# Performance work log

Measured on AMD Instinct MI355X. Metric: run time of the kernel, lower is better.

The kernel has to match this reference:

```python
import jax, jax.numpy as jnp
import numpy as np

SR = 24000
N_FFT = 2048
WIN = 960
HOP = 240
NUM_BANDS = 150
HID = 128
OUT = 64
LOG_E_MIN = -18.0  # stands in for trained log_energy_min buffer
LOG_E_MAX = 5.0    # stands in for trained log_energy_max buffer
FREQ_INTERVAL = SR / N_FFT


def _stft_power(x):
    # torchaudio Spectrogram(power=2, center=True, pad_mode=reflect)
    pad = N_FFT // 2
    xp = jnp.pad(x, ((0, 0), (pad, pad)), mode='reflect')
    n = jnp.arange(WIN, dtype=jnp.float32)
    win = 0.5 - 0.5 * jnp.cos(2.0 * jnp.pi * n / WIN)  # periodic hann
    lp = (N_FFT - WIN) // 2
    win = jnp.pad(win, (lp, N_FFT - WIN - lp))  # center-pad window to n_fft
    T = 1 + x.shape[1] // HOP
    idx = (jnp.arange(T) * HOP)[:, None] + jnp.arange(N_FFT)[None, :]  # [T, n_fft]
    frames = xp[:, idx] * win  # [B, T, n_fft]
    F = jnp.fft.rfft(frames, axis=-1)  # [B, T, n_fft//2+1]
    return F.real ** 2 + F.imag ** 2


def _lstm_dir(feat_tbd, w_ih, w_hh, b, reverse):
    # feat_tbd: [T, B, D]; PyTorch gate order i, f, g, o
    xs = jnp.flip(feat_tbd, 0) if reverse else feat_tbd
    pre = jnp.einsum('tbd,gd->tbg', xs, w_ih) + b  # input projection hoisted out of scan

    def step(carry, z_in):
        h, c = carry
        z = z_in + h @ w_hh.T
        i, f, g, o = jnp.split(z, 4, axis=-1)
        c = jax.nn.sigmoid(f) * c + jax.nn.sigmoid(i) * jnp.tanh(g)
        h = jax.nn.sigmoid(o) * jnp.tanh(c)
        return (h, c), h

    B = feat_tbd.shape[1]
    h0 = jnp.zeros((B, HID), feat_tbd.dtype)
    _, hs = jax.lax.scan(step, (h0, h0), pre)
    return jnp.flip(hs, 0) if reverse else hs


def setup_inputs() -> dict:
    key = jax.random.key(0)
    ks = jax.random.split(key, 12)
    B, L, T = 16, 240000, 1001
    x = jax.random.normal(ks[0], (B, L), jnp.float32) * 0.1
    f0_raw = jax.random.uniform(ks[1], (B, T), jnp.float32, 50.0, 400.0)
    voiced = jax.random.uniform(ks[2], (B, T)) > 0.1
    f0 = jnp.where(voiced, f0_raw, 0.0)
    D_in = NUM_BANDS * 2 + 1  # 301
    s = 0.08
    return {
        'x': x,
        'f0': f0,
        'w_ih_f': jax.random.normal(ks[3], (4 * HID, D_in), jnp.float32) * s,
        'w_hh_f': jax.random.normal(ks[4], (4 * HID, HID), jnp.float32) * s,
        'b_f': jax.random.normal(ks[5], (4 * HID,), jnp.float32) * s,
        'w_ih_b': jax.random.normal(ks[6], (4 * HID, D_in), jnp.float32) * s,
        'w_hh_b': jax.random.normal(ks[7], (4 * HID, HID), jnp.float32) * s,
        'b_b': jax.random.normal(ks[8], (4 * HID,), jnp.float32) * s,
        'ln_g': jnp.ones((2 * HID,), jnp.float32),
        'ln_b': jnp.zeros((2 * HID,), jnp.float32),
        'out_w': jax.random.normal(ks[9], (OUT, 2 * HID), jnp.float32) * 0.02,
        'out_b': jnp.zeros((OUT,), jnp.float32),
    }


def reference(x, f0, w_ih_f, w_hh_f, b_f, w_ih_b, w_hh_b, b_b, ln_g, ln_b, out_w, out_b):
    spec = _stft_power(x)                     # [B, T, 1025]
    spec = spec.at[..., -1].set(0.0)          # spec[..., -1] = 0
    Tf = min(spec.shape[1], f0.shape[1])
    spec = spec[:, :Tf]
    f0 = f0[:, :Tf]
    f0_nonzero = jnp.where(f0 > 0, f0, SR / NUM_BANDS * 0.5)
    mult = jnp.arange(1.0, NUM_BANDS + 0.5, 0.5, dtype=jnp.float32)  # [299]
    harms = f0_nonzero[..., None] * mult                              # [B, T, 299]
    harms = jnp.concatenate([harms[..., :1] * 0.5, harms], axis=-1)   # [B, T, 300]
    hidx = jnp.clip(jnp.round(harms / FREQ_INTERVAL).astype(jnp.int32), 0, spec.shape[-1] - 1)
    harms_energy = jnp.take_along_axis(spec, hidx, axis=-1)           # irregular gather
    log_energy = jnp.log(harms_energy + 1e-8)
    feature = (log_energy - LOG_E_MIN) / (LOG_E_MAX - LOG_E_MIN)
    feature = jnp.concatenate([feature, jnp.log(f0_nonzero)[..., None]], axis=-1)  # [B, T, 301]
    ft = feature.transpose(1, 0, 2)  # [T, B, 301]
    hf = _lstm_dir(ft, w_ih_f, w_hh_f, b_f, False)
    hb = _lstm_dir(ft, w_ih_b, w_hh_b, b_b, True)
    h = jnp.concatenate([hf, hb], axis=-1).transpose(1, 0, 2)  # [B, T, 256]
    mu = h.mean(-1, keepdims=True)
    var = h.var(-1, keepdims=True)
    hn = (h - mu) / jnp.sqrt(var + 1e-5) * ln_g + ln_b
    return hn @ out_w.T + out_b  # [B, T, 64]
```

## Files before the change

### kernel.cpp

```cpp
#include <hip/hip_runtime.h>

typedef __bf16 bf16x8 __attribute__((ext_vector_type(8)));
typedef float f32x4 __attribute__((ext_vector_type(4)));

__device__ __forceinline__ void sync_lds() {
    asm volatile("s_waitcnt lgkmcnt(0)" ::: "memory");
    __builtin_amdgcn_s_barrier();
}

__global__ __launch_bounds__(256) void prep_kernel(
    const float* __restrict__ x, const float* __restrict__ w_ih_f, const float* __restrict__ w_ih_b,
    __bf16* __restrict__ BT, __bf16* __restrict__ A, __bf16* __restrict__ WT)
{
    int blk = blockIdx.x;
    if (blk < 7680) {
        int id = blk * 256 + threadIdx.x;
        int n = id / 960;
        int j = id - n * 960;
        int k = n >> 1;
        int p = (k * (544 + j)) & 2047;
        float pr = (float)p * (1.0f / 2048.0f);
        float v = (n & 1) ? __builtin_amdgcn_sinf(pr) : __builtin_amdgcn_cosf(pr);
        BT[id] = (__bf16)v;
    } else if (blk < 37920) {
        int id = (blk - 7680) * 256 + threadIdx.x;
        int frame = id / 480;
        int jp = (id - frame * 480) * 2;
        float v[2] = {0.f, 0.f};
        if (frame < 16016) {
            int b = frame / 1001;
            int t = frame - b * 1001;
            const float* xb = x + (size_t)b * 240000;
            #pragma unroll
            for (int e = 0; e < 2; ++e) {
                int j = jp + e;
                int s = t * 240 + j - 480;
                if (s < 0) s = -s;
                else if (s >= 240000) s = 479998 - s;
                float win = 0.5f - 0.5f * __builtin_amdgcn_cosf((float)j * (1.0f / 960.0f));
                v[e] = xb[s] * win;
            }
        }
        union { unsigned int u; __bf16 h[2]; } pk;
        pk.h[0] = (__bf16)v[0]; pk.h[1] = (__bf16)v[1];
        *reinterpret_cast<unsigned int*>(&A[(size_t)frame * 960 + jp]) = pk.u;
    } else {
        int id = (blk - 37920) * 256 + threadIdx.x;
        int n = id / 320;
        int k = id - n * 320;
        float v = 0.f;
        if (k < 301) v = (n < 512) ? w_ih_f[n * 301 + k] : w_ih_b[(n - 512) * 301 + k];
        WT[id] = (__bf16)v;
    }
}

__global__ __launch_bounds__(256) void gemm_kernel(
    const __bf16* __restrict__ A, const __bf16* __restrict__ BT,
    int Ka, int kIters, int mode,
    __bf16* __restrict__ Cdft, float* __restrict__ pre,
    const float* __restrict__ b_f, const float* __restrict__ b_b)
{
    __shared__ __bf16 As[128 * 64];
    __shared__ __bf16 Bs[128 * 64];
    const int tid = threadIdx.x;
    const int wave = tid >> 6, lane = tid & 63, l15 = lane & 15, quad = lane >> 4;
    const int bn = blockIdx.x, bm = blockIdx.y;
    const int qm = wave >> 1, qn = wave & 1;
    f32x4 acc[4][4] = {};
    const int rl  = lane >> 3;
    const int gch = (lane & 7) ^ rl;
    const __bf16* Ag = A + (size_t)(bm * 128) * Ka;
    const __bf16* Bg = BT + (size_t)(bn * 128) * Ka;

    for (int kb = 0; kb < kIters; ++kb) {
        int k0 = kb * 64;
        #pragma unroll
        for (int p = 0; p < 4; ++p) {
            int c = wave + p * 4;
            int row = c * 8 + rl;
            __builtin_amdgcn_global_load_lds(
                (const __attribute__((address_space(1))) void*)(Ag + (size_t)row * Ka + k0 + gch * 8),
                (__attribute__((address_space(3))) void*)(As + c * 512), 16, 0, 0);
            __builtin_amdgcn_global_load_lds(
                (const __attribute__((address_space(1))) void*)(Bg + (size_t)row * Ka + k0 + gch * 8),
                (__attribute__((address_space(3))) void*)(Bs + c * 512), 16, 0, 0);
        }
        __syncthreads();
        #pragma unroll
        for (int ks = 0; ks < 2; ++ks) {
            bf16x8 af[4], bfr[4];
            #pragma unroll
            for (int i = 0; i < 4; ++i) {
                int row = qm * 64 + i * 16 + l15;
                int ch = (ks * 4 + quad) ^ (l15 & 7);
                af[i] = *reinterpret_cast<const bf16x8*>(&As[row * 64 + ch * 8]);
            }
            #pragma unroll
            for (int j = 0; j < 4; ++j) {
                int row = qn * 64 + j * 16 + l15;
                int ch = (ks * 4 + quad) ^ (l15 & 7);
                bfr[j] = *reinterpret_cast<const bf16x8*>(&Bs[row * 64 + ch * 8]);
            }
            #pragma unroll
            for (int i = 0; i < 4; ++i)
                #pragma unroll
                for (int j = 0; j < 4; ++j)
                    acc[i][j] = __builtin_amdgcn_mfma_f32_16x16x32_bf16(af[i], bfr[j], acc[i][j], 0, 0, 0);
        }
        __syncthreads();
    }

    if (mode == 0) {
        #pragma unroll
        for (int i = 0; i < 4; ++i)
            #pragma unroll
            for (int j = 0; j < 4; ++j) {
                int n = bn * 128 + qn * 64 + j * 16 + l15;
                #pragma unroll
                for (int r = 0; r < 4; ++r) {
                    int m = bm * 128 + qm * 64 + i * 16 + quad * 4 + r;
                    Cdft[(size_t)m * 2048 + n] = (__bf16)acc[i][j][r];
                }
            }
    } else {
        for (int i = 0; i < 4; ++i)
            for (int j = 0; j < 4; ++j) {
                int n = bn * 128 + qn * 64 + j * 16 + l15;
                float bias = (n < 512) ? b_f[n] : b_b[n - 512];
                int dirg = n >> 9;
                int ngate = n & 511;
                int g = ngate >> 7;
                int jj = ngate & 127;
                for (int r = 0; r < 4; ++r) {
                    int m = bm * 128 + qm * 64 + i * 16 + quad * 4 + r;
                    if (m < 16016) {
                        int b = m / 1001;
                        int t = m - b * 1001;
                        size_t off = ((size_t)(t * 2 + dirg) * 16 + b) * 512 + jj * 4 + g;
                        pre[off] = acc[i][j][r] + bias;
                    }
                }
            }
    }
}

__global__ __launch_bounds__(256) void build_feat(const float* __restrict__ f0,
    const __bf16* __restrict__ Cdft, __bf16* __restrict__ feat)
{
    __shared__ __bf16 row[2048];
    const int frame = blockIdx.x;
    const int tid = threadIdx.x;
    __builtin_amdgcn_global_load_lds(
        (const __attribute__((address_space(1))) void*)(Cdft + (size_t)frame * 2048 + tid * 8),
        (__attribute__((address_space(3))) void*)(row + (tid >> 6) * 512), 16, 0, 0);

    int b = frame / 1001;
    int t = frame - b * 1001;
    float f0v = f0[b * 1001 + t];
    float f0nz = (f0v > 0.f) ? f0v : 80.f;
    __syncthreads();

    const float LN2 = 0.6931471805599453f;
    for (int d = tid; d < 320; d += 256) {
        float val = 0.f;
        if (d < 300) {
            float mult = (d == 0) ? 0.5f : (float)(d + 1) * 0.5f;
            int kidx = (int)rintf(f0nz * mult * (1.0f / 11.71875f));
            kidx = min(max(kidx, 0), 1024);
            float e = 0.f;
            if (kidx < 1024) {
                union { unsigned int u; __bf16 h[2]; } c;
                c.u = *reinterpret_cast<const unsigned int*>(&row[2 * kidx]);
                float c0 = (float)c.h[0], c1 = (float)c.h[1];
                e = c0 * c0 + c1 * c1;
            }
            val = (__builtin_amdgcn_logf(e + 1e-8f) * LN2 + 18.f) * (1.f / 23.f);
        } else if (d == 300) {
            val = __builtin_amdgcn_logf(f0nz) * LN2;
        }
        feat[(size_t)frame * 320 + d] = (__bf16)val;
    }
}

__global__ __launch_bounds__(512, 2) void lstm_kernel(
    const float* __restrict__ w_hh_f, const float* __restrict__ w_hh_b,
    const float* __restrict__ pre, float* __restrict__ h_out)
{
    const int bid = blockIdx.x;
    const int b   = bid & 15;
    const int dir = bid >> 4;
    const float* w_hh = dir ? w_hh_b : w_hh_f;
    const int tid = threadIdx.x;
    const int wave = tid >> 6, lane = tid & 63, l15 = lane & 15, quad = lane >> 4;
    const int msel = l15 >> 2;
    const bool own = (quad == (l15 & 3));
    const int cellj = wave * 16 + l15;

    __shared__ __bf16 h_lds[2][128];

    bf16x8 afrag[4][4];
    #pragma unroll
    for (int mt = 0; mt < 4; ++mt) {
        int s = wave * 64 + mt * 16 + l15;
        const float* wrow = w_hh + (size_t)((s & 3) * 128 + (s >> 2)) * 128;
        #pragma unroll
        for (int kt = 0; kt < 4; ++kt) {
            bf16x8 v;
            #pragma unroll
            for (int e = 0; e < 8; ++e) v[e] = (__bf16)wrow[kt * 32 + quad * 8 + e];
            afrag[mt][kt] = v;
        }
    }

    if (tid < 128) h_lds[0][tid] = (__bf16)0.f;

    const int t0 = dir ? 1000 : 0;
    const ptrdiff_t pre_sstride  = dir ? -16384 : 16384;
    const ptrdiff_t hout_sstride = dir ? -2048  : 2048;
    const float* pre_base = pre + ((size_t)(t0 * 2 + dir) * 16 + b) * 512 + (size_t)cellj * 4;
    float* hout_base = h_out + (((size_t)dir * 1001 + t0) * 16 + b) * 128;

    float cstate = 0.f;
    const float L2E = 1.4426950408889634f;

    auto body = [&](int s, f32x4 P) {
        const __bf16* hb = h_lds[s & 1];
        bf16x8 bfr[4];
        #pragma unroll
        for (int kt = 0; kt < 4; ++kt)
            bfr[kt] = *reinterpret_cast<const bf16x8*>(&hb[kt * 32 + quad * 8]);

        f32x4 acc[4] = {};
        #pragma unroll
        for (int kt = 0; kt < 4; ++kt)
            #pragma unroll
            for (int mt = 0; mt < 4; ++mt)
                acc[mt] = __builtin_amdgcn_mfma_f32_16x16x32_bf16(afrag[mt][kt], bfr[kt], acc[mt], 0, 0, 0);

        f32x4 t01 = (msel & 1) ? acc[1] : acc[0];
        f32x4 t23 = (msel & 1) ? acc[3] : acc[2];
        f32x4 z4  = (msel & 2) ? t23 : t01;

        float zi = z4[0] + P[0], zf = z4[1] + P[1];
        float zg = z4[2] + P[2], zo = z4[3] + P[3];
        float A = __builtin_amdgcn_exp2f(-L2E * zi);
        float B = __builtin_amdgcn_exp2f(-L2E * zf);
        float C = __builtin_amdgcn_exp2f(-2.f * L2E * zg);
        float D = __builtin_amdgcn_exp2f(-L2E * zo);
        float Pp = (1.f + A) * (1.f + C);
        float Q = 1.f + B;
        float cn = (cstate * Pp + (1.f - C) * Q) * __builtin_amdgcn_rcpf(Pp * Q);
        if (own) cstate = cn;
        float E = __builtin_amdgcn_exp2f(-2.f * L2E * cn);
        float h = (1.f - E) * __builtin_amdgcn_rcpf((1.f + D) * (1.f + E));

        if (own) {
            h_lds[(s + 1) & 1][cellj] = (__bf16)h;
            hout_base[(ptrdiff_t)s * hout_sstride + cellj] = h;
        }
    };

    auto load_pre = [&](int sidx) -> f32x4 {
        return *reinterpret_cast<const f32x4*>(pre_base + (ptrdiff_t)sidx * pre_sstride);
    };

    f32x4 PA = load_pre(0);
    f32x4 PB = load_pre(1);
    __syncthreads();

    for (int s = 0; s < 1001; s += 2) {
        body(s, PA);
        PA = load_pre(s + 2);
        sync_lds();
        if (s + 1 < 1001) {
            body(s + 1, PB);
            PB = load_pre(s + 3);
            sync_lds();
        }
    }
}

__global__ __launch_bounds__(256) void out_kernel(
    const float* __restrict__ h_out, const float* __restrict__ ln_g, const float* __restrict__ ln_b,
    const float* __restrict__ out_w, const float* __restrict__ out_b, float* __restrict__ out)
{
    __shared__ __bf16 hn_lds[16 * 264];
    const int tid = threadIdx.x;
    const int wave = tid >> 6, lane = tid & 63, l15 = lane & 15, quad = lane >> 4;

    float lg0 = ln_g[lane],        lb0 = ln_b[lane];
    float lg1 = ln_g[64 + lane],   lb1 = ln_b[64 + lane];
    float lg2 = ln_g[128 + lane],  lb2 = ln_b[128 + lane];
    float lg3 = ln_g[192 + lane],  lb3 = ln_b[192 + lane];

    #pragma unroll
    for (int rr = 0; rr < 4; ++rr) {
        int wrow = wave * 4 + rr;
        int r = blockIdx.x * 16 + wrow;
        int b = r / 1001, t = r - b * 1001;
        size_t basef = ((size_t)t * 16 + b) * 128;
        size_t baseb = ((size_t)(1001 + t) * 16 + b) * 128;
        float h0 = h_out[basef + lane];
        float h1 = h_out[basef + 64 + lane];
        float h2 = h_out[baseb + lane];
        float h3 = h_out[baseb + 64 + lane];
        float s1 = h0 + h1 + h2 + h3;
        float s2 = h0 * h0 + h1 * h1 + h2 * h2 + h3 * h3;
        #pragma unroll
        for (int m = 32; m >= 1; m >>= 1) {
            s1 += __shfl_xor(s1, m, 64);
            s2 += __shfl_xor(s2, m, 64);
        }
        float mu = s1 * (1.f / 256.f);
        float var = s2 * (1.f / 256.f) - mu * mu;
        float rstd = rsqrtf(var + 1e-5f);
        hn_lds[wrow * 264 + lane]       = (__bf16)((h0 - mu) * rstd * lg0 + lb0);
        hn_lds[wrow * 264 + 64 + lane]  = (__bf16)((h1 - mu) * rstd * lg1 + lb1);
        hn_lds[wrow * 264 + 128 + lane] = (__bf16)((h2 - mu) * rstd * lg2 + lb2);
        hn_lds[wrow * 264 + 192 + lane] = (__bf16)((h3 - mu) * rstd * lg3 + lb3);
    }
    __syncthreads();

    const int o = wave * 16 + l15;
    f32x4 accA = {}, accB = {};
    #pragma unroll
    for (int kt = 0; kt < 8; ++kt) {
        bf16x8 a = *reinterpret_cast<const bf16x8*>(&hn_lds[l15 * 264 + kt * 32 + quad * 8]);
        const float* wp = out_w + (size_t)o * 256 + kt * 32 + quad * 8;
        bf16x8 bv;
        #pragma unroll
        for (int e = 0; e < 8; ++e) bv[e] = (__bf16)wp[e];
        if (kt & 1) accB = __builtin_amdgcn_mfma_f32_16x16x32_bf16(a, bv, accB, 0, 0, 0);
        else        accA = __builtin_amdgcn_mfma_f32_16x16x32_bf16(a, bv, accA, 0, 0, 0);
    }
    f32x4 acc = accA + accB;
    float ob = out_b[o];
    #pragma unroll
    for (int rc = 0; rc < 4; ++rc) {
        int r = blockIdx.x * 16 + quad * 4 + rc;
        out[(size_t)r * 64 + o] = acc[rc] + ob;
    }
}

extern "C" void kernel_launch(void* const* d_in, const int* in_sizes, int n_in,
                              void* d_out, int out_size, void* d_ws, size_t ws_size,
                              hipStream_t stream) {
    const float* x      = (const float*)d_in[0];
    const float* f0     = (const float*)d_in[1];
    const float* w_ih_f = (const float*)d_in[2];
    const float* w_hh_f = (const float*)d_in[3];
    const float* b_f    = (const float*)d_in[4];
    const float* w_ih_b = (const float*)d_in[5];
    const float* w_hh_b = (const float*)d_in[6];
    const float* b_b    = (const float*)d_in[7];
    const float* ln_g   = (const float*)d_in[8];
    const float* ln_b   = (const float*)d_in[9];
    const float* out_w  = (const float*)d_in[10];
    const float* out_b  = (const float*)d_in[11];
    float* out = (float*)d_out;

    char* ws = (char*)d_ws;
    size_t off = 0;
    auto alloc = [&](size_t bytes) { size_t o = off; off = (off + bytes + 255) & ~(size_t)255; return o; };
    __bf16* A     = (__bf16*)(ws + alloc((size_t)16128 * 960 * 2));
    __bf16* BT    = (__bf16*)(ws + alloc((size_t)2048 * 960 * 2));
    __bf16* Cdft  = (__bf16*)(ws + alloc((size_t)16128 * 2048 * 2));
    __bf16* feat  = (__bf16*)(ws + alloc((size_t)16128 * 320 * 2));
    __bf16* WT    = (__bf16*)(ws + alloc((size_t)1024 * 320 * 2));
    float*  preA  = (float*)(ws + alloc((size_t)(1001 * 2 + 8) * 16 * 512 * 4));
    float*  pre   = preA + (size_t)4 * 16 * 512;
    float*  h_out = (float*)(ws + alloc((size_t)2 * 1001 * 16 * 128 * 4));
    (void)ws_size; (void)in_sizes; (void)n_in; (void)out_size;

    prep_kernel <<<39200, 256, 0, stream>>>(x, w_ih_f, w_ih_b, BT, A, WT);
    gemm_kernel <<<dim3(16, 126), 256, 0, stream>>>(A, BT, 960, 15, 0, Cdft, nullptr, nullptr, nullptr);
    build_feat  <<<16016, 256, 0, stream>>>(f0, Cdft, feat);
    gemm_kernel <<<dim3(8, 126), 256, 0, stream>>>(feat, WT, 320, 5, 1, nullptr, pre, b_f, b_b);
    lstm_kernel <<<32, 512, 0, stream>>>(w_hh_f, w_hh_b, pre, h_out);
    out_kernel  <<<1001, 256, 0, stream>>>(h_out, ln_g, ln_b, out_w, out_b, out);
}
```

Baseline: 711.7 us.

## Batch four sequences per LSTM block using full MFMA N dimension

```diff
diff --git a/kernel.cpp b/kernel.cpp
--- a/kernel.cpp
+++ b/kernel.cpp
@@ -6,6 +6,10 @@
 __device__ __forceinline__ void sync_lds() {
     asm volatile("s_waitcnt lgkmcnt(0)" ::: "memory");
     __builtin_amdgcn_s_barrier();
+}
+
+__device__ __forceinline__ float swz13(float v) {
+    return __int_as_float(__builtin_amdgcn_ds_swizzle(__float_as_int(v), 0x13));
 }
 
 __global__ __launch_bounds__(256) void prep_kernel(
@@ -131,12 +135,16 @@
                 int ngate = n & 511;
                 int g = ngate >> 7;
                 int jj = ngate & 127;
+                int wv = jj >> 4;
+                int lpos = (jj & 3) * 16 + ((jj >> 2) & 3) * 4;
                 for (int r = 0; r < 4; ++r) {
                     int m = bm * 128 + qm * 64 + i * 16 + quad * 4 + r;
                     if (m < 16016) {
                         int b = m / 1001;
                         int t = m - b * 1001;
-                        size_t off = ((size_t)(t * 2 + dirg) * 16 + b) * 512 + jj * 4 + g;
+                        int grp = b >> 2, boff = b & 3;
+                        int tid_ = wv * 64 + lpos + boff;
+                        size_t off = ((((size_t)t * 2 + dirg) * 4 + grp) * 512 + tid_) * 4 + g;
                         pre[off] = acc[i][j][r] + bias;
                     }
                 }
@@ -187,16 +195,22 @@
     const float* __restrict__ pre, float* __restrict__ h_out)
 {
     const int bid = blockIdx.x;
-    const int b   = bid & 15;
-    const int dir = bid >> 4;
+    const int grp = bid & 3;
+    const int dir = bid >> 2;
     const float* w_hh = dir ? w_hh_b : w_hh_f;
     const int tid = threadIdx.x;
     const int wave = tid >> 6, lane = tid & 63, l15 = lane & 15, quad = lane >> 4;
     const int msel = l15 >> 2;
-    const bool own = (quad == (l15 & 3));
-    const int cellj = wave * 16 + l15;
-
-    __shared__ __bf16 h_lds[2][128];
+    const int nbat = l15 & 3;
+    const int cellj = wave * 16 + msel * 4 + quad;
+
+    __shared__ __bf16 h_lds[2][16 * 128];
+
+    {
+        __bf16* hz = &h_lds[0][0];
+        #pragma unroll
+        for (int i = 0; i < 8; ++i) hz[tid + i * 512] = (__bf16)0.f;
+    }
 
     bf16x8 afrag[4][4];
     #pragma unroll
@@ -212,13 +226,11 @@
         }
     }
 
-    if (tid < 128) h_lds[0][tid] = (__bf16)0.f;
-
     const int t0 = dir ? 1000 : 0;
     const ptrdiff_t pre_sstride  = dir ? -16384 : 16384;
     const ptrdiff_t hout_sstride = dir ? -2048  : 2048;
-    const float* pre_base = pre + ((size_t)(t0 * 2 + dir) * 16 + b) * 512 + (size_t)cellj * 4;
-    float* hout_base = h_out + (((size_t)dir * 1001 + t0) * 16 + b) * 128;
+    const float* pre_base = pre + ((((size_t)t0 * 2 + dir) * 4 + grp) * 512 + tid) * 4;
+    float* hout_base = h_out + (((size_t)dir * 1001 + t0) * 16 + grp * 4 + nbat) * 128 + cellj;
 
     float cstate = 0.f;
     const float L2E = 1.4426950408889634f;
@@ -227,8 +239,10 @@
         const __bf16* hb = h_lds[s & 1];
         bf16x8 bfr[4];
         #pragma unroll
-        for (int kt = 0; kt < 4; ++kt)
-            bfr[kt] = *reinterpret_cast<const bf16x8*>(&hb[kt * 32 + quad * 8]);
+        for (int kt = 0; kt < 4; ++kt) {
+            int c = (kt * 4 + quad) ^ (l15 & 7);
+            bfr[kt] = *reinterpret_cast<const bf16x8*>(&hb[l15 * 128 + c * 8]);
+        }
 
         f32x4 acc[4] = {};
         #pragma unroll
@@ -237,9 +251,21 @@
             for (int mt = 0; mt < 4; ++mt)
                 acc[mt] = __builtin_amdgcn_mfma_f32_16x16x32_bf16(afrag[mt][kt], bfr[kt], acc[mt], 0, 0, 0);
 
-        f32x4 t01 = (msel & 1) ? acc[1] : acc[0];
-        f32x4 t23 = (msel & 1) ? acc[3] : acc[2];
-        f32x4 z4  = (msel & 2) ? t23 : t01;
+        f32x4 zz0, zz1, zz2, zz3;
+        #pragma unroll
+        for (int r = 0; r < 4; ++r) {
+            zz0[r] = swz13(acc[0][r]);
+            zz1[r] = swz13(acc[1][r]);
+            zz2[r] = swz13(acc[2][r]);
+            zz3[r] = swz13(acc[3][r]);
+        }
+        f32x4 z4;
+        #pragma unroll
+        for (int r = 0; r < 4; ++r) {
+            float t01 = (msel & 1) ? zz1[r] : zz0[r];
+            float t23 = (msel & 1) ? zz3[r] : zz2[r];
+            z4[r] = (msel & 2) ? t23 : t01;
+        }
 
         float zi = z4[0] + P[0], zf = z4[1] + P[1];
         float zg = z4[2] + P[2], zo = z4[3] + P[3];
@@ -250,34 +276,29 @@
         float Pp = (1.f + A) * (1.f + C);
         float Q = 1.f + B;
         float cn = (cstate * Pp + (1.f - C) * Q) * __builtin_amdgcn_rcpf(Pp * Q);
-        if (own) cstate = cn;
+        cstate = cn;
         float E = __builtin_amdgcn_exp2f(-2.f * L2E * cn);
         float h = (1.f - E) * __builtin_amdgcn_rcpf((1.f + D) * (1.f + E));
 
-        if (own) {
-            h_lds[(s + 1) & 1][cellj] = (__bf16)h;
-            hout_base[(ptrdiff_t)s * hout_sstride + cellj] = h;
-        }
+        __bf16* hn = h_lds[(s + 1) & 1];
+        hn[nbat * 128 + (((cellj >> 3) ^ nbat) * 8) + (cellj & 7)] = (__bf16)h;
+        hout_base[(ptrdiff_t)s * hout_sstride] = h;
     };
 
     auto load_pre = [&](int sidx) -> f32x4 {
         return *reinterpret_cast<const f32x4*>(pre_base + (ptrdiff_t)sidx * pre_sstride);
     };
 
-    f32x4 PA = load_pre(0);
-    f32x4 PB = load_pre(1);
+    f32x4 P0 = load_pre(0), P1 = load_pre(1), P2 = load_pre(2), P3 = load_pre(3);
     __syncthreads();
 
-    for (int s = 0; s < 1001; s += 2) {
-        body(s, PA);
-        PA = load_pre(s + 2);
-        sync_lds();
-        if (s + 1 < 1001) {
-            body(s + 1, PB);
-            PB = load_pre(s + 3);
-            sync_lds();
-        }
-    }
+    for (int s = 0; s < 1000; s += 4) {
+        body(s, P0);     P0 = load_pre(s + 4); sync_lds();
+        body(s + 1, P1); P1 = load_pre(s + 5); sync_lds();
+        body(s + 2, P2); P2 = load_pre(s + 6); sync_lds();
+        body(s + 3, P3); P3 = load_pre(s + 7); sync_lds();
+    }
+    body(1000, P0);
 }
 
 __global__ __launch_bounds__(256) void out_kernel(
@@ -367,8 +388,8 @@
     __bf16* Cdft  = (__bf16*)(ws + alloc((size_t)16128 * 2048 * 2));
     __bf16* feat  = (__bf16*)(ws + alloc((size_t)16128 * 320 * 2));
     __bf16* WT    = (__bf16*)(ws + alloc((size_t)1024 * 320 * 2));
-    float*  preA  = (float*)(ws + alloc((size_t)(1001 * 2 + 8) * 16 * 512 * 4));
-    float*  pre   = preA + (size_t)4 * 16 * 512;
+    float*  preA  = (float*)(ws + alloc((size_t)(1001 + 16) * 16384 * 4));
+    float*  pre   = preA + (size_t)8 * 16384;
     float*  h_out = (float*)(ws + alloc((size_t)2 * 1001 * 16 * 128 * 4));
     (void)ws_size; (void)in_sizes; (void)n_in; (void)out_size;
 
@@ -376,6 +397,6 @@
     gemm_kernel <<<dim3(16, 126), 256, 0, stream>>>(A, BT, 960, 15, 0, Cdft, nullptr, nullptr, nullptr);
     build_feat  <<<16016, 256, 0, stream>>>(f0, Cdft, feat);
     gemm_kernel <<<dim3(8, 126), 256, 0, stream>>>(feat, WT, 320, 5, 1, nullptr, pre, b_f, b_b);
-    lstm_kernel <<<32, 512, 0, stream>>>(w_hh_f, w_hh_b, pre, h_out);
+    lstm_kernel <<<8, 512, 0, stream>>>(w_hh_f, w_hh_b, pre, h_out);
     out_kernel  <<<1001, 256, 0, stream>>>(h_out, ln_g, ln_b, out_w, out_b, out);
 }
```

Measured after the change: 942.0 us. 1.32x slower.
